# Optimization experiments

Measured on AMD Instinct MI355X. Metric: run time of the kernel, lower is better.

Reference implementation:

```python
import jax, jax.numpy as jnp
import numpy as np
from jax import lax

MAX_FEATURES = 50000
WIDTH = 256
EMBED = 2 * WIDTH
NUM_CLASS = 2
BATCH = 64
SEQ = 512


def setup_inputs() -> dict:
    key = jax.random.key(0)
    ks = jax.random.split(key, 10)
    s = lambda *shape: 1.0 / np.sqrt(shape[0])
    tokens = jax.random.randint(ks[0], (BATCH, SEQ), 0, MAX_FEATURES, dtype=jnp.int32)
    emb = jax.random.normal(ks[1], (MAX_FEATURES, EMBED), jnp.float32) * 0.05
    W1 = jax.random.normal(ks[2], (EMBED, WIDTH), jnp.float32) * s(EMBED)
    U1 = jax.random.normal(ks[3], (WIDTH, WIDTH), jnp.float32) * s(WIDTH)
    b1 = jnp.zeros((WIDTH,), jnp.float32)
    W2 = jax.random.normal(ks[4], (WIDTH, WIDTH), jnp.float32) * s(WIDTH)
    U2 = jax.random.normal(ks[5], (WIDTH, WIDTH), jnp.float32) * s(WIDTH)
    b2 = jnp.zeros((WIDTH,), jnp.float32)
    Wd = jax.random.normal(ks[6], (WIDTH, NUM_CLASS), jnp.float32) * s(WIDTH)
    bd = jnp.zeros((NUM_CLASS,), jnp.float32)
    return {"tokens": tokens, "emb": emb, "W1": W1, "U1": U1, "b1": b1,
            "W2": W2, "U2": U2, "b2": b2, "Wd": Wd, "bd": bd}


def _simple_rnn(x, W, U, b, return_sequences):
    # x: [B, S, D] -> precompute input projection once (big GEMM), then scan
    B = x.shape[0]
    H = U.shape[0]
    xw = jnp.einsum('bsd,dh->bsh', x, W) + b  # [B, S, H]
    def step(h, xt):
        h_new = jnp.tanh(xt + h @ U)
        return h_new, h_new
    h0 = jnp.zeros((B, H), x.dtype)
    h_last, hs = lax.scan(step, h0, jnp.swapaxes(xw, 0, 1))  # hs: [S, B, H]
    if return_sequences:
        return jnp.swapaxes(hs, 0, 1)  # [B, S, H]
    return h_last  # [B, H]


def reference(tokens, emb, W1, U1, b1, W2, U2, b2, Wd, bd):
    x = emb[tokens]                                  # [B, S, 2W] embedding lookup
    h1 = _simple_rnn(x, W1, U1, b1, return_sequences=True)   # [B, S, W]
    h2 = _simple_rnn(h1, W2, U2, b2, return_sequences=False)  # [B, W]
    logits = h2 @ Wd + bd                            # [B, num_class]
    return jax.nn.softmax(logits, axis=-1)
```

## Files before the change

### kernel.cpp

```cpp
#include <hip/hip_runtime.h>

typedef __attribute__((ext_vector_type(8))) short bf16x8;
typedef __attribute__((ext_vector_type(4))) float f32x4;

static __device__ __forceinline__ unsigned short f2bf(float x) {
    unsigned int u = __float_as_uint(x);
    u += 0x7fffu + ((u >> 16) & 1u);
    return (unsigned short)(u >> 16);
}

static __device__ __forceinline__ float selq(const f32x4* a, int q) {
    return (q == 0) ? a[0][0] : (q == 1) ? a[1][0] : (q == 2) ? a[2][0] : a[3][0];
}

static __device__ __forceinline__ void barrier_lds_only() {
    __asm__ volatile("s_waitcnt lgkmcnt(0)\n\ts_barrier" ::: "memory");
}

__global__ void transpose4(const float* __restrict__ s0, const float* __restrict__ s1,
                           const float* __restrict__ s2, const float* __restrict__ s3,
                           unsigned short* __restrict__ d0, unsigned short* __restrict__ d1,
                           unsigned short* __restrict__ d2, unsigned short* __restrict__ d3) {
    int which = blockIdx.y;
    const float* src = which == 0 ? s0 : which == 1 ? s1 : which == 2 ? s2 : s3;
    unsigned short* dst = which == 0 ? d0 : which == 1 ? d1 : which == 2 ? d2 : d3;
    int K = (which == 0) ? 512 : 256;
    int idx = blockIdx.x * 256 + threadIdx.x;
    if (idx >= K * 256) return;
    int k = idx >> 8;
    int n = idx & 255;
    dst[n * K + k] = f2bf(src[idx]);
}

template<bool GATHER>
__global__ __launch_bounds__(256, 4) void gemm_mfma(
    const void* __restrict__ Aptr, const int* __restrict__ tokens,
    const unsigned short* __restrict__ Bt, const float* __restrict__ bias,
    float* __restrict__ C, int M, int N, int K)
{
    const int bn0 = blockIdx.x * 64;
    const int m0  = blockIdx.y * 64;
    const int tid = threadIdx.x;

    __shared__ unsigned short As[64 * 40];
    __shared__ unsigned short Bs[64 * 40];
    __shared__ int tok[64];

    if (GATHER) {
        if (tid < 64) tok[tid] = tokens[m0 + tid];
        __syncthreads();
    }

    const int r  = tid >> 2;
    const int c0 = (tid & 3) * 8;
    const int w  = tid >> 6;
    const int L  = tid & 63;
    const int ml = L & 15;
    const int q  = L >> 4;
    const int kq = q * 8;

    f32x4 acc[4] = {};

    for (int k0 = 0; k0 < K; k0 += 32) {
        unsigned short tmp[8];
        if (GATHER) {
            const float* src = (const float*)Aptr + (size_t)tok[r] * K + k0 + c0;
            float4 f0 = *(const float4*)(src);
            float4 f1 = *(const float4*)(src + 4);
            tmp[0]=f2bf(f0.x); tmp[1]=f2bf(f0.y); tmp[2]=f2bf(f0.z); tmp[3]=f2bf(f0.w);
            tmp[4]=f2bf(f1.x); tmp[5]=f2bf(f1.y); tmp[6]=f2bf(f1.z); tmp[7]=f2bf(f1.w);
        } else {
            const unsigned short* src = (const unsigned short*)Aptr + (size_t)(m0 + r) * K + k0 + c0;
            *(uint4*)tmp = *(const uint4*)src;
        }
        *(uint4*)&As[r * 40 + c0] = *(const uint4*)tmp;
        *(uint4*)&Bs[r * 40 + c0] = *(const uint4*)(Bt + (size_t)(bn0 + r) * K + k0 + c0);
        __syncthreads();

        bf16x8 av = *(const bf16x8*)&As[(16 * w + ml) * 40 + kq];
#pragma unroll
        for (int ns = 0; ns < 4; ++ns) {
            bf16x8 bv = *(const bf16x8*)&Bs[(ns * 16 + ml) * 40 + kq];
            acc[ns] = __builtin_amdgcn_mfma_f32_16x16x32_bf16(av, bv, acc[ns], 0, 0, 0);
        }
        __syncthreads();
    }

#pragma unroll
    for (int ns = 0; ns < 4; ++ns) {
        int gn = bn0 + ns * 16 + ml;
        float bv = bias[gn];
#pragma unroll
        for (int rr = 0; rr < 4; ++rr) {
            int gm = m0 + 16 * w + q * 4 + rr;
            C[(size_t)gm * N + gn] = acc[ns][rr] + bv;
        }
    }
}

__global__ __launch_bounds__(512) void rnn_pipe(
    float* xw,
    const unsigned short* __restrict__ U1t,
    const unsigned short* __restrict__ W2t,
    const unsigned short* __restrict__ U2t,
    const float* __restrict__ b2,
    int* flags,
    float* __restrict__ out_last)
{
    const int bid = blockIdx.x;
    const int tid = threadIdx.x;
    const int w   = tid >> 6;
    const int rw  = w & 3;
    const int L   = tid & 63;
    const int col = tid & 255;
    const int q   = L >> 4;
    const int ml  = L & 15;

    __shared__ unsigned short hsh[2][256];

    if (bid < 64) {
        const int b = bid;
        int* flagp = flags + b;

        bf16x8 Bf[4][8];
        const unsigned short* Bsrc = (w < 4) ? U1t : W2t;
#pragma unroll
        for (int i = 0; i < 4; ++i) {
            const unsigned short* up = Bsrc + (size_t)((rw * 4 + i) * 16 + ml) * 256 + q * 8;
#pragma unroll
            for (int kt = 0; kt < 8; ++kt)
                Bf[i][kt] = *(const bf16x8*)(up + kt * 32);
        }
        if (tid < 256) hsh[0][tid] = 0;

        const float* xb  = xw + (size_t)b * 512 * 256 + col;
        const float* xpf = xb + 4 * 256;
        float xq0 = 0.f, xq1 = 0.f, xq2 = 0.f, xq3 = 0.f;
        if (w < 4) { xq0 = xb[0]; xq1 = xb[256]; xq2 = xb[512]; xq3 = xb[768]; }
        const float b2c = (w >= 4) ? b2[col] : 0.f;
        float* pst = xw + ((size_t)b * 512 * 256 + col) - 256;
        __syncthreads();

#define PTICK(RP, XQ, PF, ST)                                                        \
    {                                                                                \
        if (w < 4) {                                                                 \
            bf16x8 af[8];                                                            \
            _Pragma("unroll")                                                        \
            for (int kt = 0; kt < 8; ++kt)                                           \
                af[kt] = *(const bf16x8*)&hsh[RP][kt * 32 + q * 8];                  \
            float xnew = 0.f;                                                        \
            if (PF) { xnew = *xpf; xpf += 256; }                                     \
            f32x4 accA[4] = {}, accB[4] = {};                                        \
            _Pragma("unroll")                                                        \
            for (int kt = 0; kt < 8; kt += 2) {                                      \
                _Pragma("unroll")                                                    \
                for (int i = 0; i < 4; ++i)                                          \
                    accA[i] = __builtin_amdgcn_mfma_f32_16x16x32_bf16(af[kt], Bf[i][kt], accA[i], 0, 0, 0);       \
                _Pragma("unroll")                                                    \
                for (int i = 0; i < 4; ++i)                                          \
                    accB[i] = __builtin_amdgcn_mfma_f32_16x16x32_bf16(af[kt + 1], Bf[i][kt + 1], accB[i], 0, 0, 0); \
            }                                                                        \
            float z  = selq(accA, q) + selq(accB, q) + XQ;                           \
            float e  = __expf(2.f * z);              \
            float hn = 1.f - 2.f * __builtin_amdgcn_rcpf(e + 1.f);                   \
            hsh[(RP) ^ 1][col] = f2bf(hn);                                           \
            XQ = xnew;                                                               \
        } else {                                                                     \
            if (ST) {                                                                \
                bf16x8 af[8];                                                        \
                _Pragma("unroll")                                                    \
                for (int kt = 0; kt < 8; ++kt)                                       \
                    af[kt] = *(const bf16x8*)&hsh[RP][kt * 32 + q * 8];              \
                f32x4 aWA[4] = {}, aWB[4] = {};                                      \
                _Pragma("unroll")                                                    \
                for (int kt = 0; kt < 8; kt += 2) {                                  \
                    _Pragma("unroll")                                                \
                    for (int i = 0; i < 4; ++i)                                      \
                        aWA[i] = __builtin_amdgcn_mfma_f32_16x16x32_bf16(af[kt], Bf[i][kt], aWA[i], 0, 0, 0);       \
                    _Pragma("unroll")                                                \
                    for (int i = 0; i < 4; ++i)                                      \
                        aWB[i] = __builtin_amdgcn_mfma_f32_16x16x32_bf16(af[kt + 1], Bf[i][kt + 1], aWB[i], 0, 0, 0); \
                }                                                                    \
                *pst = selq(aWA, q) + selq(aWB, q) + b2c;                            \
            }                                                                        \
            pst += 256;                                                              \
        }                                                                            \
        barrier_lds_only();                                                          \
    }

        PTICK(0, xq0, 1, 0) PTICK(1, xq1, 1, 1) PTICK(0, xq2, 1, 1) PTICK(1, xq3, 1, 1)
        PTICK(0, xq0, 1, 1) PTICK(1, xq1, 1, 1) PTICK(0, xq2, 1, 1) PTICK(1, xq3, 1, 1)
        asm volatile("s_waitcnt vmcnt(0)" ::: "memory");
        __builtin_amdgcn_s_barrier();
        if (tid == 0)
            __hip_atomic_store(flagp, 7, __ATOMIC_RELEASE, __HIP_MEMORY_SCOPE_AGENT);

        for (int g = 1; g < 63; ++g) {
            PTICK(0, xq0, 1, 1) PTICK(1, xq1, 1, 1) PTICK(0, xq2, 1, 1) PTICK(1, xq3, 1, 1)
            PTICK(0, xq0, 1, 1) PTICK(1, xq1, 1, 1) PTICK(0, xq2, 1, 1) PTICK(1, xq3, 1, 1)
            asm volatile("s_waitcnt vmcnt(0)" ::: "memory");
            __builtin_amdgcn_s_barrier();
            if (tid == 0)
                __hip_atomic_store(flagp, 8 * g + 7, __ATOMIC_RELEASE, __HIP_MEMORY_SCOPE_AGENT);
        }
        PTICK(0, xq0, 1, 1) PTICK(1, xq1, 1, 1) PTICK(0, xq2, 1, 1) PTICK(1, xq3, 1, 1)
        PTICK(0, xq0, 0, 1) PTICK(1, xq1, 0, 1) PTICK(0, xq2, 0, 1) PTICK(1, xq3, 0, 1)
        if (w >= 4) {
            bf16x8 af[8];
#pragma unroll
            for (int kt = 0; kt < 8; ++kt)
                af[kt] = *(const bf16x8*)&hsh[0][kt * 32 + q * 8];
            f32x4 aWA[4] = {}, aWB[4] = {};
#pragma unroll
            for (int kt = 0; kt < 8; kt += 2) {
#pragma unroll
                for (int i = 0; i < 4; ++i)
                    aWA[i] = __builtin_amdgcn_mfma_f32_16x16x32_bf16(af[kt], Bf[i][kt], aWA[i], 0, 0, 0);
#pragma unroll
                for (int i = 0; i < 4; ++i)
                    aWB[i] = __builtin_amdgcn_mfma_f32_16x16x32_bf16(af[kt + 1], Bf[i][kt + 1], aWB[i], 0, 0, 0);
            }
            *pst = selq(aWA, q) + selq(aWB, q) + b2c;
        }
        barrier_lds_only();
        asm volatile("s_waitcnt vmcnt(0)" ::: "memory");
        __builtin_amdgcn_s_barrier();
        if (tid == 0)
            __hip_atomic_store(flagp, 1024, __ATOMIC_RELEASE, __HIP_MEMORY_SCOPE_AGENT);
#undef PTICK

    } else {
        const int b = bid - 64;
        int* flagp = flags + b;

        bf16x8 Bf[4][8];
#pragma unroll
        for (int i = 0; i < 4; ++i) {
            const unsigned short* up = U2t + (size_t)((rw * 4 + i) * 16 + ml) * 256 + q * 8;
#pragma unroll
            for (int kt = 0; kt < 8; ++kt)
                Bf[i][kt] = *(const bf16x8*)(up + kt * 32);
        }
        if (tid < 256) hsh[0][tid] = 0;
        const float* pbc = xw + (size_t)b * 512 * 256 + col;
        float lastv = 0.f;
        __syncthreads();

#define CTICK(RP, PV)                                                                \
    {                                                                                \
        if (w < 4) {                                                                 \
            bf16x8 af[8];                                                            \
            _Pragma("unroll")                                                        \
            for (int kt = 0; kt < 8; ++kt)                                           \
                af[kt] = *(const bf16x8*)&hsh[RP][kt * 32 + q * 8];                  \
            f32x4 accA[4] = {}, accB[4] = {};                                        \
            _Pragma("unroll")                                                        \
            for (int kt = 0; kt < 8; kt += 2) {                                      \
                _Pragma("unroll")                                                    \
                for (int i = 0; i < 4; ++i)                                          \
                    accA[i] = __builtin_amdgcn_mfma_f32_16x16x32_bf16(af[kt], Bf[i][kt], accA[i], 0, 0, 0);       \
                _Pragma("unroll")                                                    \
                for (int i = 0; i < 4; ++i)                                          \
                    accB[i] = __builtin_amdgcn_mfma_f32_16x16x32_bf16(af[kt + 1], Bf[i][kt + 1], accB[i], 0, 0, 0); \
            }                                                                        \
            float z  = selq(accA, q) + selq(accB, q) + (PV);                         \
            float e  = __expf(2.f * z);                                              \
            float hn = 1.f - 2.f * __builtin_amdgcn_rcpf(e + 1.f);                   \
            lastv = hn;                                                              \
            hsh[(RP) ^ 1][col] = f2bf(hn);                                           \
        }                                                                            \
        barrier_lds_only();                                                          \
    }

        for (int c = 0; c < 32; ++c) {
            const int t0 = c * 16;
            if (tid == 0) {
                int it = 0;
                while (__hip_atomic_load(flagp, __ATOMIC_ACQUIRE, __HIP_MEMORY_SCOPE_AGENT) < t0 + 16) {
                    __builtin_amdgcn_s_sleep(2);
                    if (++it > (1 << 17)) break;
                }
            }
            __syncthreads();
            float pv[16];
            if (w < 4) {
#pragma unroll
                for (int j = 0; j < 16; ++j)
                    pv[j] = pbc[(size_t)(t0 + j) << 8];
            }
            CTICK(0, pv[0])  CTICK(1, pv[1])  CTICK(0, pv[2])  CTICK(1, pv[3])
            CTICK(0, pv[4])  CTICK(1, pv[5])  CTICK(0, pv[6])  CTICK(1, pv[7])
            CTICK(0, pv[8])  CTICK(1, pv[9])  CTICK(0, pv[10]) CTICK(1, pv[11])
            CTICK(0, pv[12]) CTICK(1, pv[13]) CTICK(0, pv[14]) CTICK(1, pv[15])
        }
#undef CTICK

        if (w < 4) out_last[b * 256 + col] = lastv;
    }
}

__global__ void head_kernel(const float* __restrict__ h2, const float* __restrict__ Wd,
                            const float* __restrict__ bd, float* __restrict__ out)
{
    int tid = threadIdx.x;
    int b = tid >> 1, c = tid & 1;
    float s = bd[c];
    for (int jj = 0; jj < 256; ++jj) s = fmaf(h2[b * 256 + jj], Wd[jj * 2 + c], s);
    __shared__ float lg[128];
    lg[tid] = s;
    __syncthreads();
    float o0 = lg[b * 2 + 0], o1 = lg[b * 2 + 1];
    float m = fmaxf(o0, o1);
    float z = __expf(o0 - m) + __expf(o1 - m);
    out[tid] = __expf(s - m) * __builtin_amdgcn_rcpf(z);
}

extern "C" void kernel_launch(void* const* d_in, const int* in_sizes, int n_in,
                              void* d_out, int out_size, void* d_ws, size_t ws_size,
                              hipStream_t stream) {
    const int*   tokens = (const int*)d_in[0];
    const float* emb    = (const float*)d_in[1];
    const float* W1     = (const float*)d_in[2];
    const float* U1     = (const float*)d_in[3];
    const float* b1     = (const float*)d_in[4];
    const float* W2     = (const float*)d_in[5];
    const float* U2     = (const float*)d_in[6];
    const float* b2     = (const float*)d_in[7];
    const float* Wd     = (const float*)d_in[8];
    const float* bd     = (const float*)d_in[9];
    float* out = (float*)d_out;

    char* ws = (char*)d_ws;
    float*          xw  = (float*)ws;
    char*           p   = ws + 33554432 + 16777216;
    unsigned short* W1t = (unsigned short*)p;            p += 512 * 256 * 2;
    unsigned short* W2t = (unsigned short*)p;            p += 256 * 256 * 2;
    unsigned short* U1t = (unsigned short*)p;            p += 256 * 256 * 2;
    unsigned short* U2t = (unsigned short*)p;            p += 256 * 256 * 2;
    float*          h2  = (float*)p;                     p += 64 * 256 * 4;
    int*            flags = (int*)p;

    const int M = 64 * 512;

    hipMemsetAsync(flags, 0, 64 * sizeof(int), stream);

    transpose4<<<dim3(512, 4), 256, 0, stream>>>(W1, W2, U1, U2, W1t, W2t, U1t, U2t);

    gemm_mfma<true><<<dim3(256 / 64, M / 64), 256, 0, stream>>>(
        emb, tokens, W1t, b1, xw, M, 256, 512);

    rnn_pipe<<<128, 512, 0, stream>>>(xw, U1t, W2t, U2t, b2, flags, h2);

    head_kernel<<<1, 128, 0, stream>>>(h2, Wd, bd, out);
}
```

Baseline: 620.8 us.

## Batch layer-2 input projection over 16-step LDS ring and prefetch GEMM loads

The producer block now keeps a 32-slot LDS ring of hidden states, so the W2 projection waves run one batched 16-row MFMA pass every 16 steps instead of a tiny per-step projection. The flag to the consumer block is published once per 16-step group. Separately, the input GEMM loads the next K tile into registers before the MFMA work on the current one. This cuts the per-step work of the projection waves and hides GEMM load latency, but publishes progress less often, which can add latency at the consumer.

```diff
diff --git a/kernel.cpp b/kernel.cpp
--- a/kernel.cpp
+++ b/kernel.cpp
@@ -46,11 +46,6 @@
     __shared__ unsigned short Bs[64 * 40];
     __shared__ int tok[64];
 
-    if (GATHER) {
-        if (tid < 64) tok[tid] = tokens[m0 + tid];
-        __syncthreads();
-    }
-
     const int r  = tid >> 2;
     const int c0 = (tid & 3) * 8;
     const int w  = tid >> 6;
@@ -59,23 +54,41 @@
     const int q  = L >> 4;
     const int kq = q * 8;
 
+    if (GATHER) {
+        if (tid < 64) tok[tid] = tokens[m0 + tid];
+        __syncthreads();
+    }
+
+    const float* af32 = nullptr;
+    const unsigned short* abf = nullptr;
+    if (GATHER) af32 = (const float*)Aptr + (size_t)tok[r] * K + c0;
+    else        abf  = (const unsigned short*)Aptr + (size_t)(m0 + r) * K + c0;
+    const unsigned short* bsrc = Bt + (size_t)(bn0 + r) * K + c0;
+
+    float4 f0, f1; uint4 ab, bb;
+    if (GATHER) { f0 = *(const float4*)af32; f1 = *(const float4*)(af32 + 4); af32 += 32; }
+    else        { ab = *(const uint4*)abf; abf += 32; }
+    bb = *(const uint4*)bsrc; bsrc += 32;
+
     f32x4 acc[4] = {};
 
     for (int k0 = 0; k0 < K; k0 += 32) {
         unsigned short tmp[8];
         if (GATHER) {
-            const float* src = (const float*)Aptr + (size_t)tok[r] * K + k0 + c0;
-            float4 f0 = *(const float4*)(src);
-            float4 f1 = *(const float4*)(src + 4);
             tmp[0]=f2bf(f0.x); tmp[1]=f2bf(f0.y); tmp[2]=f2bf(f0.z); tmp[3]=f2bf(f0.w);
             tmp[4]=f2bf(f1.x); tmp[5]=f2bf(f1.y); tmp[6]=f2bf(f1.z); tmp[7]=f2bf(f1.w);
         } else {
-            const unsigned short* src = (const unsigned short*)Aptr + (size_t)(m0 + r) * K + k0 + c0;
-            *(uint4*)tmp = *(const uint4*)src;
+            *(uint4*)tmp = ab;
         }
         *(uint4*)&As[r * 40 + c0] = *(const uint4*)tmp;
-        *(uint4*)&Bs[r * 40 + c0] = *(const uint4*)(Bt + (size_t)(bn0 + r) * K + k0 + c0);
-        __syncthreads();
+        *(uint4*)&Bs[r * 40 + c0] = bb;
+        __syncthreads();
+
+        if (k0 + 32 < K) {
+            if (GATHER) { f0 = *(const float4*)af32; f1 = *(const float4*)(af32 + 4); af32 += 32; }
+            else        { ab = *(const uint4*)abf; abf += 32; }
+            bb = *(const uint4*)bsrc; bsrc += 32;
+        }
 
         bf16x8 av = *(const bf16x8*)&As[(16 * w + ml) * 40 + kq];
 #pragma unroll
@@ -116,7 +129,7 @@
     const int q   = L >> 4;
     const int ml  = L & 15;
 
-    __shared__ unsigned short hsh[2][256];
+    __shared__ unsigned short ring[32][256];
 
     if (bid < 64) {
         const int b = bid;
@@ -131,107 +144,103 @@
             for (int kt = 0; kt < 8; ++kt)
                 Bf[i][kt] = *(const bf16x8*)(up + kt * 32);
         }
-        if (tid < 256) hsh[0][tid] = 0;
-
-        const float* xb  = xw + (size_t)b * 512 * 256 + col;
-        const float* xpf = xb + 4 * 256;
-        float xq0 = 0.f, xq1 = 0.f, xq2 = 0.f, xq3 = 0.f;
-        if (w < 4) { xq0 = xb[0]; xq1 = xb[256]; xq2 = xb[512]; xq3 = xb[768]; }
-        const float b2c = (w >= 4) ? b2[col] : 0.f;
-        float* pst = xw + ((size_t)b * 512 * 256 + col) - 256;
-        __syncthreads();
-
-#define PTICK(RP, XQ, PF, ST)                                                        \
-    {                                                                                \
-        if (w < 4) {                                                                 \
-            bf16x8 af[8];                                                            \
-            _Pragma("unroll")                                                        \
-            for (int kt = 0; kt < 8; ++kt)                                           \
-                af[kt] = *(const bf16x8*)&hsh[RP][kt * 32 + q * 8];                  \
-            float xnew = 0.f;                                                        \
-            if (PF) { xnew = *xpf; xpf += 256; }                                     \
-            f32x4 accA[4] = {}, accB[4] = {};                                        \
-            _Pragma("unroll")                                                        \
-            for (int kt = 0; kt < 8; kt += 2) {                                      \
-                _Pragma("unroll")                                                    \
-                for (int i = 0; i < 4; ++i)                                          \
-                    accA[i] = __builtin_amdgcn_mfma_f32_16x16x32_bf16(af[kt], Bf[i][kt], accA[i], 0, 0, 0);       \
-                _Pragma("unroll")                                                    \
-                for (int i = 0; i < 4; ++i)                                          \
-                    accB[i] = __builtin_amdgcn_mfma_f32_16x16x32_bf16(af[kt + 1], Bf[i][kt + 1], accB[i], 0, 0, 0); \
-            }                                                                        \
-            float z  = selq(accA, q) + selq(accB, q) + XQ;                           \
-            float e  = __expf(2.f * z);              \
-            float hn = 1.f - 2.f * __builtin_amdgcn_rcpf(e + 1.f);                   \
-            hsh[(RP) ^ 1][col] = f2bf(hn);                                           \
-            XQ = xnew;                                                               \
-        } else {                                                                     \
-            if (ST) {                                                                \
-                bf16x8 af[8];                                                        \
-                _Pragma("unroll")                                                    \
-                for (int kt = 0; kt < 8; ++kt)                                       \
-                    af[kt] = *(const bf16x8*)&hsh[RP][kt * 32 + q * 8];              \
-                f32x4 aWA[4] = {}, aWB[4] = {};                                      \
-                _Pragma("unroll")                                                    \
-                for (int kt = 0; kt < 8; kt += 2) {                                  \
-                    _Pragma("unroll")                                                \
-                    for (int i = 0; i < 4; ++i)                                      \
-                        aWA[i] = __builtin_amdgcn_mfma_f32_16x16x32_bf16(af[kt], Bf[i][kt], aWA[i], 0, 0, 0);       \
-                    _Pragma("unroll")                                                \
-                    for (int i = 0; i < 4; ++i)                                      \
-                        aWB[i] = __builtin_amdgcn_mfma_f32_16x16x32_bf16(af[kt + 1], Bf[i][kt + 1], aWB[i], 0, 0, 0); \
-                }                                                                    \
-                *pst = selq(aWA, q) + selq(aWB, q) + b2c;                            \
-            }                                                                        \
-            pst += 256;                                                              \
-        }                                                                            \
-        barrier_lds_only();                                                          \
-    }
-
-        PTICK(0, xq0, 1, 0) PTICK(1, xq1, 1, 1) PTICK(0, xq2, 1, 1) PTICK(1, xq3, 1, 1)
-        PTICK(0, xq0, 1, 1) PTICK(1, xq1, 1, 1) PTICK(0, xq2, 1, 1) PTICK(1, xq3, 1, 1)
-        asm volatile("s_waitcnt vmcnt(0)" ::: "memory");
+        if (tid < 256) ring[31][tid] = 0;
+
+        const float* xpf = xw + (size_t)b * 512 * 256 + col;
+        float xq[4];
+        float b2v[4];
+        if (w < 4) {
+            xq[0] = xpf[0]; xq[1] = xpf[256]; xq[2] = xpf[512]; xq[3] = xpf[768];
+            xpf += 4 * 256;
+        } else {
+#pragma unroll
+            for (int i = 0; i < 4; ++i) b2v[i] = b2[rw * 64 + i * 16 + ml];
+        }
+        float* pb = xw + (size_t)b * 512 * 256;
+        __syncthreads();
+
+        for (int g = 0; g < 32; ++g) {
+            const int half = g & 1;
+#pragma unroll
+            for (int j = 0; j < 16; ++j) {
+                if (w < 4) {
+                    const int slot_r = (j == 0) ? ((half ^ 1) * 16 + 15) : (half * 16 + j - 1);
+                    bf16x8 af[8];
+#pragma unroll
+                    for (int kt = 0; kt < 8; ++kt)
+                        af[kt] = *(const bf16x8*)&ring[slot_r][kt * 32 + q * 8];
+                    float xnew = *xpf; xpf += 256;
+                    f32x4 accA[4] = {}, accB[4] = {};
+#pragma unroll
+                    for (int kt = 0; kt < 8; kt += 2) {
+#pragma unroll
+                        for (int i = 0; i < 4; ++i)
+                            accA[i] = __builtin_amdgcn_mfma_f32_16x16x32_bf16(af[kt], Bf[i][kt], accA[i], 0, 0, 0);
+#pragma unroll
+                        for (int i = 0; i < 4; ++i)
+                            accB[i] = __builtin_amdgcn_mfma_f32_16x16x32_bf16(af[kt + 1], Bf[i][kt + 1], accB[i], 0, 0, 0);
+                    }
+                    float z  = selq(accA, q) + selq(accB, q) + xq[j & 3];
+                    float e  = __expf(2.f * z);
+                    float hn = 1.f - 2.f * __builtin_amdgcn_rcpf(e + 1.f);
+                    ring[half * 16 + j][col] = f2bf(hn);
+                    xq[j & 3] = xnew;
+                } else {
+                    if (j == 0 && g > 0) {
+                        const int half2 = half ^ 1;
+                        const int t0 = (g - 1) * 16;
+                        bf16x8 af[8];
+#pragma unroll
+                        for (int kt = 0; kt < 8; ++kt)
+                            af[kt] = *(const bf16x8*)&ring[half2 * 16 + ml][kt * 32 + q * 8];
+                        f32x4 acc[4] = {};
+#pragma unroll
+                        for (int kt = 0; kt < 8; ++kt)
+#pragma unroll
+                            for (int i = 0; i < 4; ++i)
+                                acc[i] = __builtin_amdgcn_mfma_f32_16x16x32_bf16(af[kt], Bf[i][kt], acc[i], 0, 0, 0);
+                        float* ps = pb + (size_t)t0 * 256 + q * 1024 + rw * 64 + ml;
+#pragma unroll
+                        for (int i = 0; i < 4; ++i)
+#pragma unroll
+                            for (int rr = 0; rr < 4; ++rr)
+                                ps[rr * 256 + i * 16] = acc[i][rr] + b2v[i];
+                    }
+                    if (j == 8 && g > 0)
+                        asm volatile("s_waitcnt vmcnt(0)" ::: "memory");
+                }
+                if (j == 9 && g > 0 && tid == 0)
+                    __hip_atomic_store(flagp, 16 * g, __ATOMIC_RELEASE, __HIP_MEMORY_SCOPE_AGENT);
+                barrier_lds_only();
+            }
+        }
+        if (w >= 4) {
+            bf16x8 af[8];
+#pragma unroll
+            for (int kt = 0; kt < 8; ++kt)
+                af[kt] = *(const bf16x8*)&ring[16 + ml][kt * 32 + q * 8];
+            f32x4 acc[4] = {};
+#pragma unroll
+            for (int kt = 0; kt < 8; ++kt)
+#pragma unroll
+                for (int i = 0; i < 4; ++i)
+                    acc[i] = __builtin_amdgcn_mfma_f32_16x16x32_bf16(af[kt], Bf[i][kt], acc[i], 0, 0, 0);
+            float* ps = pb + (size_t)496 * 256 + q * 1024 + rw * 64 + ml;
+#pragma unroll
+            for (int i = 0; i < 4; ++i)
+#pragma unroll
+                for (int rr = 0; rr < 4; ++rr)
+                    ps[rr * 256 + i * 16] = acc[i][rr] + b2v[i];
+            asm volatile("s_waitcnt vmcnt(0)" ::: "memory");
+        }
         __builtin_amdgcn_s_barrier();
         if (tid == 0)
-            __hip_atomic_store(flagp, 7, __ATOMIC_RELEASE, __HIP_MEMORY_SCOPE_AGENT);
-
-        for (int g = 1; g < 63; ++g) {
-            PTICK(0, xq0, 1, 1) PTICK(1, xq1, 1, 1) PTICK(0, xq2, 1, 1) PTICK(1, xq3, 1, 1)
-            PTICK(0, xq0, 1, 1) PTICK(1, xq1, 1, 1) PTICK(0, xq2, 1, 1) PTICK(1, xq3, 1, 1)
-            asm volatile("s_waitcnt vmcnt(0)" ::: "memory");
-            __builtin_amdgcn_s_barrier();
-            if (tid == 0)
-                __hip_atomic_store(flagp, 8 * g + 7, __ATOMIC_RELEASE, __HIP_MEMORY_SCOPE_AGENT);
-        }
-        PTICK(0, xq0, 1, 1) PTICK(1, xq1, 1, 1) PTICK(0, xq2, 1, 1) PTICK(1, xq3, 1, 1)
-        PTICK(0, xq0, 0, 1) PTICK(1, xq1, 0, 1) PTICK(0, xq2, 0, 1) PTICK(1, xq3, 0, 1)
-        if (w >= 4) {
-            bf16x8 af[8];
-#pragma unroll
-            for (int kt = 0; kt < 8; ++kt)
-                af[kt] = *(const bf16x8*)&hsh[0][kt * 32 + q * 8];
-            f32x4 aWA[4] = {}, aWB[4] = {};
-#pragma unroll
-            for (int kt = 0; kt < 8; kt += 2) {
-#pragma unroll
-                for (int i = 0; i < 4; ++i)
-                    aWA[i] = __builtin_amdgcn_mfma_f32_16x16x32_bf16(af[kt], Bf[i][kt], aWA[i], 0, 0, 0);
-#pragma unroll
-                for (int i = 0; i < 4; ++i)
-                    aWB[i] = __builtin_amdgcn_mfma_f32_16x16x32_bf16(af[kt + 1], Bf[i][kt + 1], aWB[i], 0, 0, 0);
-            }
-            *pst = selq(aWA, q) + selq(aWB, q) + b2c;
-        }
-        barrier_lds_only();
-        asm volatile("s_waitcnt vmcnt(0)" ::: "memory");
-        __builtin_amdgcn_s_barrier();
-        if (tid == 0)
-            __hip_atomic_store(flagp, 1024, __ATOMIC_RELEASE, __HIP_MEMORY_SCOPE_AGENT);
-#undef PTICK
+            __hip_atomic_store(flagp, 512, __ATOMIC_RELEASE, __HIP_MEMORY_SCOPE_AGENT);
 
     } else {
         const int b = bid - 64;
         int* flagp = flags + b;
+        unsigned short (*hsh)[256] = ring;
 
         bf16x8 Bf[4][8];
 #pragma unroll
```

After: 547.4 us. -11.8%, faster.
